# Kernel tuning notes

Measured on AMD Instinct MI355X. Metric: run time of the kernel, lower is better.

The kernel has to match this reference:

```python
import jax, jax.numpy as jnp
import numpy as np

B, W, D = 8, 1024, 1024
HEADS, KDIM, VDIM = 16, 64, 64


def setup_inputs() -> dict:
    key = jax.random.key(0)
    k1, k2, k3, k4 = jax.random.split(key, 4)
    # he_normal-ish scaling for weights
    s = (2.0 / D) ** 0.5
    return {
        "inputs": jax.random.normal(k1, (B, W, D), dtype=jnp.float32),
        "Wq": jax.random.normal(k2, (D, HEADS * KDIM), dtype=jnp.float32) * s,
        "Wk": jax.random.normal(k3, (D, HEADS * KDIM), dtype=jnp.float32) * s,
        "Wv": jax.random.normal(k4, (D, HEADS * VDIM), dtype=jnp.float32) * s,
    }


def reference(inputs, Wq, Wk, Wv):
    # Self-attention: memory = inputs
    bsz, win, _ = inputs.shape
    # DenseHeads: linear projection, reshaped to (B, W, heads, head_units)
    q = (inputs @ Wq).reshape(bsz, win, HEADS, KDIM)
    k = (inputs @ Wk).reshape(bsz, win, HEADS, KDIM)
    v = (inputs @ Wv).reshape(bsz, win, HEADS, VDIM)
    scale = KDIM ** (-0.5)
    # scores[b,q,h,m] = sum_k Q[b,q,h,k] * K[b,m,h,k]
    scores = jnp.einsum("bqhk,bmhk->bqhm", q, k) * scale
    attn = jax.nn.softmax(scores, axis=-1)
    # out[b,q,h,v] = sum_m attn[b,q,h,m] * V[b,m,h,v]
    out = jnp.einsum("bqhm,bmhv->bqhv", attn, v)
    return out
```

## Files before the change

### kernel.cpp

```cpp
#include <hip/hip_runtime.h>
#include <stdint.h>


using bf16x8 = __attribute__((ext_vector_type(8))) __bf16;
using f32x4  = __attribute__((ext_vector_type(4))) float;
using f16x4  = __attribute__((ext_vector_type(4))) _Float16;

union frag_u  { uint4 u4; bf16x8 f; };
union vfrag_u { uint2 u2; f16x4 f; };
union pfrag_u { unsigned int u[2]; f16x4 f; };

__device__ inline unsigned short f2bf(float x){
  unsigned int u = __float_as_uint(x);
  u += 0x7fffu + ((u >> 16) & 1u);
  return (unsigned short)(u >> 16);
}

__device__ inline unsigned int pkrtz_u32(float a, float b){
  auto r = __builtin_amdgcn_cvt_pkrtz(a, b);
  unsigned int u; __builtin_memcpy(&u, &r, 4); return u;
}

__device__ inline void gl_lds16(const void* g, void* l){
  __builtin_amdgcn_global_load_lds(
      (const __attribute__((address_space(1))) void*)g,
      (__attribute__((address_space(3))) void*)l, 16, 0, 0);
}

__global__ void cast_all(const float* __restrict__ X,
                         const float* __restrict__ Wq, const float* __restrict__ Wk,
                         const float* __restrict__ Wv,
                         unsigned short* __restrict__ Xb,
                         unsigned short* __restrict__ Wt){
  __shared__ float tile[64][65];
  int bid = blockIdx.x;
  if (bid < 8192){
    int i = (bid * 256 + threadIdx.x) * 4;
    float4 v = *(const float4*)(X + i);
    ushort4 o;
    o.x = f2bf(v.x); o.y = f2bf(v.y); o.z = f2bf(v.z); o.w = f2bf(v.w);
    *(ushort4*)(Xb + i) = o;
    return;
  }
  int id = bid - 8192;
  int proj = id >> 8;
  int rem  = id & 255;
  int kt = rem & 15, nt = rem >> 4;
  const float* Wsrc = (proj == 0) ? Wq : ((proj == 1) ? Wk : Wv);
  int k0 = kt * 64, n0 = nt * 64;
  int tx = threadIdx.x & 63, ty = threadIdx.x >> 6;
  for (int i = 0; i < 16; i++){
    int k = i * 4 + ty;
    tile[k][tx] = Wsrc[(k0 + k) * 1024 + n0 + tx];
  }
  __syncthreads();
  for (int i = 0; i < 16; i++){
    int n = i * 4 + ty;
    Wt[(proj * 1024 + n0 + n) * 1024 + k0 + tx] = f2bf(tile[tx][n]);
  }
}

__global__ void gemm_qkv(const unsigned short* __restrict__ Xb,
                         const unsigned short* __restrict__ Wt,
                         unsigned short* __restrict__ QK,
                         unsigned short* __restrict__ Vt){
  __shared__ __align__(16) unsigned short Abuf[128 * 64];
  __shared__ __align__(16) unsigned short Bbuf[128 * 64];
  int bid = blockIdx.x;
  int bx = bid >> 6, by = bid & 63;
  int w = threadIdx.x >> 6, lane = threadIdx.x & 63;
  int g = lane >> 4, li = lane & 15;
  int lrow = lane >> 3, lcol = lane & 7;
  int wm = (w >> 1) * 64, wn = (w & 1) * 64;
  f32x4 acc[4][4] = {};

  for (int k0 = 0; k0 < 1024; k0 += 64){
    __syncthreads();
    for (int i = 0; i < 4; i++){
      int idx = w * 4 + i;
      int row = idx * 8 + lrow;
      gl_lds16(Xb + (by * 128 + row) * 1024 + k0 + lcol * 8, Abuf + idx * 512);
      gl_lds16(Wt + (bx * 128 + row) * 1024 + k0 + lcol * 8, Bbuf + idx * 512);
    }
    __syncthreads();
    for (int c = 0; c < 2; c++){
      frag_u a[4], b[4];
      for (int i = 0; i < 4; i++)
        a[i].u4 = *(const uint4*)(Abuf + (wm + i * 16 + li) * 64 + c * 32 + g * 8);
      for (int j = 0; j < 4; j++)
        b[j].u4 = *(const uint4*)(Bbuf + (wn + j * 16 + li) * 64 + c * 32 + g * 8);
      for (int i = 0; i < 4; i++)
        for (int j = 0; j < 4; j++)
          acc[i][j] = __builtin_amdgcn_mfma_f32_16x16x32_bf16(a[i].f, b[j].f, acc[i][j], 0, 0, 0);
    }
  }
  if (bx >= 16){
    for (int i = 0; i < 4; i++){
      int row = by * 128 + wm + i * 16 + g * 4;
      int bb = row >> 10, m = row & 1023;
      for (int j = 0; j < 4; j++){
        int vc = bx * 128 + wn + j * 16 + li - 2048;
        int hh = vc >> 6, dd = vc & 63;
        uint2 cv;
        cv.x = pkrtz_u32(acc[i][j][0], acc[i][j][1]);
        cv.y = pkrtz_u32(acc[i][j][2], acc[i][j][3]);
        *(uint2*)(Vt + ((size_t)(bb * 16 + hh) * 64 + dd) * 1024 + m) = cv;
      }
    }
  } else {
    float sc = (bx < 8) ? 0.1803368801111f : 1.0f;
    for (int i = 0; i < 4; i++){
      int row = by * 128 + wm + i * 16 + g * 4;
      for (int j = 0; j < 4; j++){
        int col = bx * 128 + wn + j * 16 + li;
        for (int r = 0; r < 4; r++)
          QK[(size_t)(row + r) * 2048 + col] = f2bf(acc[i][j][r] * sc);
      }
    }
  }
}

__global__ __launch_bounds__(256, 4) void attn(const unsigned short* __restrict__ QK,
                                               const unsigned short* __restrict__ Vt,
                                               float* __restrict__ Out){
  __shared__ __align__(16) unsigned short Kbuf[64 * 64];
  __shared__ __align__(16) unsigned short Vbuf[64 * 64];
  int id = blockIdx.x;
  int bh = id & 127, qb = id >> 7;
  int b = bh >> 4, h = bh & 15;
  int w = threadIdx.x >> 6, lane = threadIdx.x & 63;
  int g = lane >> 4, li = lane & 15;
  int lrow = lane >> 3, lcol = lane & 7;
  int scol = ((lcol ^ lrow) & 7) * 8;

  frag_u qf[2];
  {
    int tok = b * 1024 + qb * 64 + w * 16 + li;
    const unsigned short* qp = QK + (size_t)tok * 2048 + h * 64 + g * 8;
    qf[0].u4 = *(const uint4*)(qp);
    qf[1].u4 = *(const uint4*)(qp + 32);
  }

  f32x4 o[4] = {};
  f32x4 osum = {};
  const f32x4 bias = {-10.f, -10.f, -10.f, -10.f};
  pfrag_u ones;
  ones.u[0] = 0x3c003c00u; ones.u[1] = 0x3c003c00u;

  const unsigned short* Kg = QK + (size_t)b * 1024 * 2048 + 1024 + h * 64;
  const unsigned short* Vg = Vt + (size_t)bh * 65536;

  for (int mt = 0; mt < 16; mt++){
    int m0 = mt * 64;
    __syncthreads();
    for (int i = 0; i < 2; i++){
      int idx = w * 2 + i;
      int row = idx * 8 + lrow;
      gl_lds16(Kg + (size_t)(m0 + row) * 2048 + scol, Kbuf + idx * 512);
      gl_lds16(Vg + row * 1024 + m0 + scol,           Vbuf + idx * 512);
    }
    __syncthreads();

    f32x4 s[4];
    for (int t = 0; t < 4; t++) s[t] = bias;
    for (int t = 0; t < 4; t++){
      for (int c = 0; c < 2; c++){
        frag_u kf;
        kf.u4 = *(const uint4*)(Kbuf + (t * 16 + li) * 64 + ((((c << 2) + g) ^ (li & 7)) << 3));
        s[t] = __builtin_amdgcn_mfma_f32_16x16x32_bf16(kf.f, qf[c].f, s[t], 0, 0, 0);
      }
    }

    pfrag_u pf[4];
    for (int t = 0; t < 4; t++){
      float p0 = __builtin_exp2f(s[t][0]);
      float p1 = __builtin_exp2f(s[t][1]);
      float p2 = __builtin_exp2f(s[t][2]);
      float p3 = __builtin_exp2f(s[t][3]);
      pf[t].u[0] = pkrtz_u32(p0, p1);
      pf[t].u[1] = pkrtz_u32(p2, p3);
    }

    for (int t = 0; t < 4; t++)
      osum = __builtin_amdgcn_mfma_f32_16x16x16f16(ones.f, pf[t].f, osum, 0, 0, 0);
    for (int tv = 0; tv < 4; tv++){
      for (int t = 0; t < 4; t++){
        int gg = ((t * 2 + (g >> 1)) ^ (li & 7));
        vfrag_u vf;
        vf.u2 = *(const uint2*)(Vbuf + (tv * 16 + li) * 64 + gg * 8 + (g & 1) * 4);
        o[tv] = __builtin_amdgcn_mfma_f32_16x16x16f16(vf.f, pf[t].f, o[tv], 0, 0, 0);
      }
    }
  }

  float inv = 1.f / osum[0];

  int tok = b * 1024 + qb * 64 + w * 16 + li;
  float* op = Out + (size_t)tok * 1024 + h * 64 + g * 4;
  for (int tv = 0; tv < 4; tv++){
    float4 v4;
    v4.x = o[tv][0] * inv; v4.y = o[tv][1] * inv;
    v4.z = o[tv][2] * inv; v4.w = o[tv][3] * inv;
    *(float4*)(op + tv * 16) = v4;
  }
}

extern "C" void kernel_launch(void* const* d_in, const int* in_sizes, int n_in,
                              void* d_out, int out_size, void* d_ws, size_t ws_size,
                              hipStream_t stream) {
  const float* X  = (const float*)d_in[0];
  const float* Wq = (const float*)d_in[1];
  const float* Wk = (const float*)d_in[2];
  const float* Wv = (const float*)d_in[3];
  float* Out = (float*)d_out;
  char* ws = (char*)d_ws;
  unsigned short* Xb = (unsigned short*)(ws);
  unsigned short* Wt = (unsigned short*)(ws + (size_t)16 * 1024 * 1024);
  unsigned short* QK = (unsigned short*)(ws + (size_t)22 * 1024 * 1024);
  unsigned short* Vt = (unsigned short*)(ws + (size_t)54 * 1024 * 1024);

  cast_all<<<8960, 256, 0, stream>>>(X, Wq, Wk, Wv, Xb, Wt);
  gemm_qkv<<<1536, 256, 0, stream>>>(Xb, Wt, QK, Vt);
  attn    <<<2048, 256, 0, stream>>>(QK, Vt, Out);
}
```

Before: 213.9 us.

## Rewrite QKV GEMM with 256x192 tiles, double-buffered LDS prefetch and swizzle

Replaces the 128x128 QKV projection GEMM with a 512-thread, 256x192-tile kernel. It double-buffers the A and B LDS tiles, prefetches the next K slice through direct global-to-LDS loads interleaved with the MFMA phases, uses XOR-swizzled LDS addressing, raises MFMA priority with setprio, and remaps blocks for grid locality. The goal is to hide global load latency, cut LDS bank conflicts and barrier stalls, and improve operand reuse. In exchange it relies on hand-placed waitcnt and barrier choreography that must be exactly right, and on heavier register and LDS use.

```diff
diff --git a/kernel.cpp b/kernel.cpp
--- a/kernel.cpp
+++ b/kernel.cpp
@@ -26,6 +26,10 @@
       (const __attribute__((address_space(1))) void*)g,
       (__attribute__((address_space(3))) void*)l, 16, 0, 0);
 }
+
+#define SBAR() do{ asm volatile("" ::: "memory"); __builtin_amdgcn_s_barrier(); asm volatile("" ::: "memory"); }while(0)
+#define LGKM0() asm volatile("s_waitcnt lgkmcnt(0)" ::: "memory")
+#define VMC(n)  asm volatile("s_waitcnt vmcnt(" #n ")" ::: "memory")
 
 __global__ void cast_all(const float* __restrict__ X,
                          const float* __restrict__ Wq, const float* __restrict__ Wk,
@@ -60,64 +64,138 @@
   }
 }
 
-__global__ void gemm_qkv(const unsigned short* __restrict__ Xb,
-                         const unsigned short* __restrict__ Wt,
-                         unsigned short* __restrict__ QK,
-                         unsigned short* __restrict__ Vt){
-  __shared__ __align__(16) unsigned short Abuf[128 * 64];
-  __shared__ __align__(16) unsigned short Bbuf[128 * 64];
+
+__device__ __forceinline__ void tile_step(
+    const unsigned short* __restrict__ Xb,
+    const unsigned short* __restrict__ Wt,
+    const char* Ab, const char* Bb, char* AbN, char* BbS,
+    const int* aoff, const int* boff, int t, int w,
+    int aRdS, int bRdS, f32x4 acc[8][3])
+{
+  frag_u bfr[3][2];
+#pragma unroll
+  for (int n = 0; n < 3; n++)
+#pragma unroll
+    for (int kk = 0; kk < 2; kk++)
+      bfr[n][kk].u4 = *(const uint4*)(Bb + bRdS + n * 2048 + kk * 64);
+
+#pragma unroll
+  for (int p = 0; p < 4; p++){
+    frag_u afr[2][2];
+#pragma unroll
+    for (int i = 0; i < 2; i++)
+#pragma unroll
+      for (int kk = 0; kk < 2; kk++)
+        afr[i][kk].u4 = *(const uint4*)(Ab + aRdS + (p * 2 + i) * 2048 + kk * 64);
+    if (p == 0){
+      gl_lds16(Xb + aoff[0] + (t + 1) * 64, AbN + (0 * 8 + w) * 1024);
+      gl_lds16(Xb + aoff[1] + (t + 1) * 64, AbN + (1 * 8 + w) * 1024);
+    } else if (p == 1){
+      gl_lds16(Xb + aoff[2] + (t + 1) * 64, AbN + (2 * 8 + w) * 1024);
+      gl_lds16(Xb + aoff[3] + (t + 1) * 64, AbN + (3 * 8 + w) * 1024);
+    } else if (p == 2){
+      gl_lds16(Wt + boff[0] + (t + 2) * 64, BbS + (0 * 8 + w) * 1024);
+      gl_lds16(Wt + boff[1] + (t + 2) * 64, BbS + (1 * 8 + w) * 1024);
+    } else {
+      gl_lds16(Wt + boff[2] + (t + 2) * 64, BbS + (2 * 8 + w) * 1024);
+    }
+    SBAR();
+    LGKM0();
+    __builtin_amdgcn_s_setprio(1);
+#pragma unroll
+    for (int kk = 0; kk < 2; kk++)
+#pragma unroll
+      for (int i = 0; i < 2; i++)
+#pragma unroll
+        for (int n = 0; n < 3; n++)
+          acc[p * 2 + i][n] = __builtin_amdgcn_mfma_f32_16x16x32_bf16(
+              afr[i][kk].f, bfr[n][kk].f, acc[p * 2 + i][n], 0, 0, 0);
+    __builtin_amdgcn_s_setprio(0);
+    if (p == 3) VMC(3);
+    SBAR();
+  }
+}
+
+__global__ __launch_bounds__(512, 2) void gemm_qkv(
+    const unsigned short* __restrict__ Xb,
+    const unsigned short* __restrict__ Wt,
+    unsigned short* __restrict__ QK,
+    unsigned short* __restrict__ Vt){
+  __shared__ __align__(16) char Abuf[2][32768];
+  __shared__ __align__(16) char Bbuf[2][24576];
+
   int bid = blockIdx.x;
-  int bx = bid >> 6, by = bid & 63;
-  int w = threadIdx.x >> 6, lane = threadIdx.x & 63;
-  int g = lane >> 4, li = lane & 15;
-  int lrow = lane >> 3, lcol = lane & 7;
-  int wm = (w >> 1) * 64, wn = (w & 1) * 64;
-  f32x4 acc[4][4] = {};
-
-  for (int k0 = 0; k0 < 1024; k0 += 64){
-    __syncthreads();
-    for (int i = 0; i < 4; i++){
-      int idx = w * 4 + i;
-      int row = idx * 8 + lrow;
-      gl_lds16(Xb + (by * 128 + row) * 1024 + k0 + lcol * 8, Abuf + idx * 512);
-      gl_lds16(Wt + (bx * 128 + row) * 1024 + k0 + lcol * 8, Bbuf + idx * 512);
-    }
-    __syncthreads();
-    for (int c = 0; c < 2; c++){
-      frag_u a[4], b[4];
-      for (int i = 0; i < 4; i++)
-        a[i].u4 = *(const uint4*)(Abuf + (wm + i * 16 + li) * 64 + c * 32 + g * 8);
-      for (int j = 0; j < 4; j++)
-        b[j].u4 = *(const uint4*)(Bbuf + (wn + j * 16 + li) * 64 + c * 32 + g * 8);
-      for (int i = 0; i < 4; i++)
-        for (int j = 0; j < 4; j++)
-          acc[i][j] = __builtin_amdgcn_mfma_f32_16x16x32_bf16(a[i].f, b[j].f, acc[i][j], 0, 0, 0);
-    }
-  }
-  if (bx >= 16){
-    for (int i = 0; i < 4; i++){
-      int row = by * 128 + wm + i * 16 + g * 4;
-      int bb = row >> 10, m = row & 1023;
-      for (int j = 0; j < 4; j++){
-        int vc = bx * 128 + wn + j * 16 + li - 2048;
-        int hh = vc >> 6, dd = vc & 63;
+  int tau = (bid & 7) * 64 + (bid >> 3);
+  int by = tau >> 4, bx = tau & 15;
+  int tid = threadIdx.x;
+  int w = tid >> 6, lane = tid & 63;
+  int li = lane & 15, g = lane >> 4;
+  int wr = w >> 2, wc = w & 3;
+
+  int aoff[4], boff[3];
+#pragma unroll
+  for (int j = 0; j < 4; j++){
+    int s = ((j * 8 + w) << 10) + (lane << 4);
+    int p = s ^ (((s >> 9) & 1) << 5);
+    aoff[j] = (by * 256 + (p >> 7)) * 1024 + ((p & 127) >> 1);
+  }
+#pragma unroll
+  for (int j = 0; j < 3; j++){
+    int s = ((j * 8 + w) << 10) + (lane << 4);
+    int p = s ^ (((s >> 9) & 1) << 5);
+    boff[j] = (bx * 192 + (p >> 7)) * 1024 + ((p & 127) >> 1);
+  }
+  int swzbit = ((li >> 2) & 1) << 5;
+  int aRdS = ((wr * 128 + li) * 128 + g * 16) ^ swzbit;
+  int bRdS = ((wc * 48  + li) * 128 + g * 16) ^ swzbit;
+
+  f32x4 acc[8][3] = {};
+
+  gl_lds16(Wt + boff[0], Bbuf[0] + (0 * 8 + w) * 1024);
+  gl_lds16(Wt + boff[1], Bbuf[0] + (1 * 8 + w) * 1024);
+  gl_lds16(Wt + boff[2], Bbuf[0] + (2 * 8 + w) * 1024);
+#pragma unroll
+  for (int j = 0; j < 4; j++)
+    gl_lds16(Xb + aoff[j], Abuf[0] + (j * 8 + w) * 1024);
+  gl_lds16(Wt + boff[0] + 64, Bbuf[1] + (0 * 8 + w) * 1024);
+  gl_lds16(Wt + boff[1] + 64, Bbuf[1] + (1 * 8 + w) * 1024);
+  gl_lds16(Wt + boff[2] + 64, Bbuf[1] + (2 * 8 + w) * 1024);
+  VMC(3);
+  SBAR();
+
+  for (int t = 0; t < 16; t += 2){
+    tile_step(Xb, Wt, Abuf[0], Bbuf[0], Abuf[1], Bbuf[0], aoff, boff, t,     w, aRdS, bRdS, acc);
+    tile_step(Xb, Wt, Abuf[1], Bbuf[1], Abuf[0], Bbuf[1], aoff, boff, t + 1, w, aRdS, bRdS, acc);
+  }
+
+  int row0 = by * 256 + wr * 128 + g * 4;
+  int bb16 = (by >> 2) * 16;
+#pragma unroll
+  for (int n = 0; n < 3; n++){
+    int cb = bx * 192 + wc * 48 + n * 16;
+    if (cb < 2048){
+      float sc = (cb < 1024) ? 0.1803368801111f : 1.0f;
+#pragma unroll
+      for (int m = 0; m < 8; m++){
+        int row = row0 + m * 16;
+#pragma unroll
+        for (int r = 0; r < 4; r++)
+          QK[(size_t)(row + r) * 2048 + cb + li] = f2bf(acc[m][n][r] * sc);
+      }
+    } else {
+      int vc = cb + li - 2048;
+      int hh = vc >> 6, dd = vc & 63;
+#pragma unroll
+      for (int m = 0; m < 8; m++){
+        int mtok = (row0 + m * 16) & 1023;
         uint2 cv;
-        cv.x = pkrtz_u32(acc[i][j][0], acc[i][j][1]);
-        cv.y = pkrtz_u32(acc[i][j][2], acc[i][j][3]);
-        *(uint2*)(Vt + ((size_t)(bb * 16 + hh) * 64 + dd) * 1024 + m) = cv;
+        cv.x = pkrtz_u32(acc[m][n][0], acc[m][n][1]);
+        cv.y = pkrtz_u32(acc[m][n][2], acc[m][n][3]);
+        *(uint2*)(Vt + ((size_t)(bb16 + hh) * 64 + dd) * 1024 + mtok) = cv;
       }
     }
-  } else {
-    float sc = (bx < 8) ? 0.1803368801111f : 1.0f;
-    for (int i = 0; i < 4; i++){
-      int row = by * 128 + wm + i * 16 + g * 4;
-      for (int j = 0; j < 4; j++){
-        int col = bx * 128 + wn + j * 16 + li;
-        for (int r = 0; r < 4; r++)
-          QK[(size_t)(row + r) * 2048 + col] = f2bf(acc[i][j][r] * sc);
-      }
-    }
-  }
+  }
+  VMC(0);
 }
 
 __global__ __launch_bounds__(256, 4) void attn(const unsigned short* __restrict__ QK,
@@ -220,6 +298,6 @@
   unsigned short* Vt = (unsigned short*)(ws + (size_t)54 * 1024 * 1024);
 
   cast_all<<<8960, 256, 0, stream>>>(X, Wq, Wk, Wv, Xb, Wt);
-  gemm_qkv<<<1536, 256, 0, stream>>>(Xb, Wt, QK, Vt);
+  gemm_qkv<<<512, 512, 0, stream>>>(Xb, Wt, QK, Vt);
   attn    <<<2048, 256, 0, stream>>>(QK, Vt, Out);
 }
```

New measurement: 213.0 us. About the same (-0.4%).
